# Kernel optimization log

Measured on AMD Instinct MI355X. Metric: run time of the kernel, lower is better.

Reference implementation:

```python
import jax, jax.numpy as jnp
from jax import lax
import numpy as np

IN, HID, OUT = 28, 64, 10


def _lstm_layer(x_seq, W_ih, W_hh, b_ih, b_hh):
    # x_seq: [B, T, in]; PyTorch gate order: i, f, g, o (stacked along 4H)
    B = x_seq.shape[0]
    H = W_hh.shape[1]
    # Precompute input projection for all timesteps: [B, T, 4H]
    x_proj = jnp.einsum('bti,gi->btg', x_seq, W_ih) + b_ih + b_hh

    def step(carry, xt):
        h, c = carry
        gates = xt + h @ W_hh.T  # [B, 4H]
        i, f, g, o = jnp.split(gates, 4, axis=-1)
        i = jax.nn.sigmoid(i)
        f = jax.nn.sigmoid(f)
        g = jnp.tanh(g)
        o = jax.nn.sigmoid(o)
        c = f * c + i * g
        h = o * jnp.tanh(c)
        return (h, c), h

    h0 = jnp.zeros((B, H), x_seq.dtype)
    (_, _), hs = lax.scan(step, (h0, h0), jnp.swapaxes(x_proj, 0, 1))
    return jnp.swapaxes(hs, 0, 1)  # [B, T, H]


def setup_inputs() -> dict:
    key = jax.random.key(0)
    ks = jax.random.split(key, 12)
    s_in = 1.0 / np.sqrt(HID)
    u = lambda k, shape: jax.random.uniform(k, shape, jnp.float32, -s_in, s_in)
    return {
        'x': jax.random.normal(ks[0], (16384, 1, 28, 28), jnp.float32),
        'W_ih0': u(ks[1], (4 * HID, IN)),
        'W_hh0': u(ks[2], (4 * HID, HID)),
        'b_ih0': u(ks[3], (4 * HID,)),
        'b_hh0': u(ks[4], (4 * HID,)),
        'W_ih1': u(ks[5], (4 * HID, HID)),
        'W_hh1': u(ks[6], (4 * HID, HID)),
        'b_ih1': u(ks[7], (4 * HID,)),
        'b_hh1': u(ks[8], (4 * HID,)),
        'W_lin': u(ks[9], (OUT, HID)),
        'b_lin': u(ks[10], (OUT,)),
    }


def reference(x, W_ih0, W_hh0, b_ih0, b_hh0, W_ih1, W_hh1, b_ih1, b_hh1, W_lin, b_lin):
    # (N, C, H, W) -> (N, C*H, W): sequence of rows, feature = W = 28
    x = x.reshape(x.shape[0], -1, x.shape[-1])
    h1 = _lstm_layer(x, W_ih0, W_hh0, b_ih0, b_hh0)   # [B, T, 64]
    h2 = _lstm_layer(h1, W_ih1, W_hh1, b_ih1, b_hh1)  # [B, T, 64]
    last = h2[:, -1, :]
    return last @ W_lin.T + b_lin  # [B, 10]
```

## Files before the change

### kernel.cpp

```cpp
#include <hip/hip_runtime.h>


typedef _Float16 half8 __attribute__((ext_vector_type(8)));
typedef float floatx4 __attribute__((ext_vector_type(4)));

#define NFRAG 112
#define WS_BIAS_OFF (NFRAG * 1024)
#define K2 2.8853900817779268f

#if __has_builtin(__builtin_amdgcn_exp2f)
#define EXP2(v) __builtin_amdgcn_exp2f(v)
#else
#define EXP2(v) __expf(0.6931471805599453f * (v))
#endif
#define RCP(v) __builtin_amdgcn_rcpf(v)

__global__ void prep_kernel(const float* __restrict__ Wih0, const float* __restrict__ Whh0,
                            const float* __restrict__ bih0, const float* __restrict__ bhh0,
                            const float* __restrict__ Wih1, const float* __restrict__ Whh1,
                            const float* __restrict__ bih1, const float* __restrict__ bhh1,
                            _Float16* __restrict__ wA, float* __restrict__ wBias) {
    int idx = blockIdx.x * blockDim.x + threadIdx.x;
    if (idx < NFRAG * 512) {
        int f = idx >> 9, slot = idx & 511;
        int lane = slot >> 3, j = slot & 7;
        int mt, kt, layer;
        if (f < 48) { layer = 0; mt = f / 3; kt = f % 3; }
        else        { layer = 1; int f2 = f - 48; mt = f2 >> 2; kt = f2 & 3; }
        int m = mt * 16 + (lane & 15);
        int k = kt * 32 + (lane >> 4) * 8 + j;
        int u = m >> 2, g = m & 3;
        int row = g * 64 + u;
        float v;
        if (layer == 0) {
            if (k < 28)       v = Wih0[row * 28 + k];
            else if (k == 28) v = bih0[row] + bhh0[row];
            else if (k < 32)  v = 0.f;
            else              v = Whh0[row * 64 + (k - 32)];
        } else {
            if (k < 64)       v = Wih1[row * 64 + k];
            else              v = Whh1[row * 64 + (k - 64)];
        }
        float s = (g == 2) ? K2 : -1.4426950408889634f;
        wA[idx] = (_Float16)(v * s);
    } else if (idx < NFRAG * 512 + 256) {
        int m = idx - NFRAG * 512;
        int g = m & 3;
        int row = g * 64 + (m >> 2);
        float s = (g == 2) ? K2 : -1.4426950408889634f;
        wBias[m] = (bih1[row] + bhh1[row]) * s;
    }
}

template <int N>
__device__ __forceinline__ void gate_batch(const floatx4* acc, float* c,
                                           _Float16* const* planes, const int* offs) {
    float ei[N], ef[N], eg[N], eo[N];
    #pragma unroll
    for (int i = 0; i < N; ++i) {
        floatx4 a = acc[i];
        ei[i] = EXP2(a[0]);
        ef[i] = EXP2(a[1]);
        eg[i] = EXP2(a[2]);
        eo[i] = EXP2(a[3]);
    }
    float num[N], rd[N], po[N];
    #pragma unroll
    for (int i = 0; i < N; ++i) {
        float pi = 1.0f + ei[i];
        float pf = 1.0f + ef[i];
        float pg = 1.0f + eg[i];
        po[i] = 1.0f + eo[i];
        float m = pg * pi;
        num[i] = c[i] * m + (eg[i] - 1.0f) * pf;
        rd[i]  = RCP(pf * m);
    }
    float ec[N];
    #pragma unroll
    for (int i = 0; i < N; ++i) {
        float cn = num[i] * rd[i];
        c[i] = cn;
        ec[i] = EXP2(K2 * cn);
    }
    #pragma unroll
    for (int i = 0; i < N; ++i) {
        float r2 = RCP(ec[i] * po[i] + po[i]);
        float h = (ec[i] - 1.0f) * r2;
        planes[i][offs[i]] = (_Float16)h;
    }
}

__launch_bounds__(512, 4)
__global__ void lstm_mfma(const float* __restrict__ x,
                          const _Float16* __restrict__ wA,
                          const float* __restrict__ wBias,
                          const float* __restrict__ Wlin, const float* __restrict__ blin,
                          float* __restrict__ out) {
    __shared__ __align__(16) _Float16 h0p[2][2048];
    __shared__ __align__(16) _Float16 h1p[2][2048];
    __shared__ __align__(16) _Float16 xb[2][1024];
    __shared__ float wlin_s[640];
    __shared__ float blin_s[10];

    const int lane = threadIdx.x;
    const int w    = threadIdx.y;
    const int tid  = w * 64 + lane;
    const int quad = lane >> 4;
    const int col  = lane & 15;

    half8 A0[2][3], A1[2][4];
    floatx4 bias1[2];
    int hwr[2][2];
    #pragma unroll
    for (int j = 0; j < 2; ++j) {
        const int MT = 2 * w + j;
        #pragma unroll
        for (int kt = 0; kt < 3; ++kt)
            A0[j][kt] = *(const half8*)(wA + (MT * 3 + kt) * 512 + lane * 8);
        #pragma unroll
        for (int kt = 0; kt < 4; ++kt)
            A1[j][kt] = *(const half8*)(wA + (48 + MT * 4 + kt) * 512 + lane * 8);
        const int u = MT * 4 + quad;
        bias1[j] = *(const floatx4*)(wBias + u * 4);
        #pragma unroll
        for (int in = 0; in < 2; ++in)
            hwr[j][in] = (in * 2 + (u >> 5)) * 512 + (((u >> 3) & 3) * 16 + col) * 8 + (u & 7);
    }

    int xrd[2], hrd[2][2];
    #pragma unroll
    for (int in = 0; in < 2; ++in) {
        xrd[in] = in * 512 + lane * 8;
        #pragma unroll
        for (int kt = 0; kt < 2; ++kt) hrd[kt][in] = (in * 2 + kt) * 512 + lane * 8;
    }

    const int xi = tid & 31;
    const bool xvalid = xi < 28;
    const int xbi = tid >> 5;
    const float* xg = x + (blockIdx.x * 32 + xbi) * 784 + xi;
    const int xstg = ((xi >> 3) * 16 + xbi) * 8 + (xi & 7);

    {
        ((int*)&h0p[1][0])[tid * 2 + 0] = 0;
        ((int*)&h0p[1][0])[tid * 2 + 1] = 0;
        ((int*)&h1p[1][0])[tid * 2 + 0] = 0;
        ((int*)&h1p[1][0])[tid * 2 + 1] = 0;
        float xv0 = xvalid ? xg[0] : 0.f;
        float xv1 = xvalid ? xg[16 * 784] : 0.f;
        xb[0][xstg]       = (xi == 28) ? (_Float16)1.0f : (_Float16)xv0;
        xb[0][xstg + 512] = (xi == 28) ? (_Float16)1.0f : (_Float16)xv1;
    }
    __syncthreads();

    float c0[2][2] = {{0.f, 0.f}, {0.f, 0.f}};
    float c1[2][2] = {{0.f, 0.f}, {0.f, 0.f}};

    for (int p = -1; p <= 27; ++p) {
        const int pr  = p & 1;
        const int pr1 = pr ^ 1;
        const bool doL0 = (p < 27);
        const bool doL1 = (p >= 0);

        float xn0 = 0.f, xn1 = 0.f;
        if (p <= 25 && xvalid) {
            xn0 = xg[(p + 2) * 28];
            xn1 = xg[16 * 784 + (p + 2) * 28];
        }

        half8 bx[2], bh0[2][2];
        if (doL0) {
            #pragma unroll
            for (int in = 0; in < 2; ++in)
                bx[in] = *(const half8*)&xb[pr1][xrd[in]];
        }
        #pragma unroll
        for (int kt = 0; kt < 2; ++kt)
            #pragma unroll
            for (int in = 0; in < 2; ++in)
                bh0[kt][in] = *(const half8*)&h0p[pr][hrd[kt][in]];

        floatx4 acc0[2][2], acc1[2][2];
        if (doL0) {
            #pragma unroll
            for (int j = 0; j < 2; ++j)
                #pragma unroll
                for (int in = 0; in < 2; ++in) {
                    acc0[j][in] = __builtin_amdgcn_mfma_f32_16x16x32_f16(
                                      A0[j][0], bx[in], (floatx4){0.f, 0.f, 0.f, 0.f}, 0, 0, 0);
                    #pragma unroll
                    for (int kt = 0; kt < 2; ++kt)
                        acc0[j][in] = __builtin_amdgcn_mfma_f32_16x16x32_f16(
                                          A0[j][kt + 1], bh0[kt][in], acc0[j][in], 0, 0, 0);
                }
        }
        if (doL1) {
            #pragma unroll
            for (int j = 0; j < 2; ++j)
                #pragma unroll
                for (int in = 0; in < 2; ++in) {
                    acc1[j][in] = bias1[j];
                    #pragma unroll
                    for (int kt = 0; kt < 2; ++kt)
                        acc1[j][in] = __builtin_amdgcn_mfma_f32_16x16x32_f16(
                                          A1[j][kt], bh0[kt][in], acc1[j][in], 0, 0, 0);
                }

            half8 bh1[2][2];
            #pragma unroll
            for (int kt = 0; kt < 2; ++kt)
                #pragma unroll
                for (int in = 0; in < 2; ++in)
                    bh1[kt][in] = *(const half8*)&h1p[pr1][hrd[kt][in]];
            #pragma unroll
            for (int j = 0; j < 2; ++j)
                #pragma unroll
                for (int kt = 0; kt < 2; ++kt)
                    #pragma unroll
                    for (int in = 0; in < 2; ++in)
                        acc1[j][in] = __builtin_amdgcn_mfma_f32_16x16x32_f16(
                                          A1[j][kt + 2], bh1[kt][in], acc1[j][in], 0, 0, 0);
        }

        if (doL0 && doL1) {
            floatx4 a8[8] = {acc0[0][0], acc0[0][1], acc0[1][0], acc0[1][1],
                             acc1[0][0], acc1[0][1], acc1[1][0], acc1[1][1]};
            float   cc[8] = {c0[0][0], c0[0][1], c0[1][0], c0[1][1],
                             c1[0][0], c1[0][1], c1[1][0], c1[1][1]};
            _Float16* pl[8] = {h0p[pr1], h0p[pr1], h0p[pr1], h0p[pr1],
                               h1p[pr],  h1p[pr],  h1p[pr],  h1p[pr]};
            int offs[8] = {hwr[0][0], hwr[0][1], hwr[1][0], hwr[1][1],
                           hwr[0][0], hwr[0][1], hwr[1][0], hwr[1][1]};
            gate_batch<8>(a8, cc, pl, offs);
            c0[0][0] = cc[0]; c0[0][1] = cc[1]; c0[1][0] = cc[2]; c0[1][1] = cc[3];
            c1[0][0] = cc[4]; c1[0][1] = cc[5]; c1[1][0] = cc[6]; c1[1][1] = cc[7];
        } else if (doL0) {
            floatx4 a4[4] = {acc0[0][0], acc0[0][1], acc0[1][0], acc0[1][1]};
            float   cc[4] = {c0[0][0], c0[0][1], c0[1][0], c0[1][1]};
            _Float16* pl[4] = {h0p[pr1], h0p[pr1], h0p[pr1], h0p[pr1]};
            int offs[4] = {hwr[0][0], hwr[0][1], hwr[1][0], hwr[1][1]};
            gate_batch<4>(a4, cc, pl, offs);
            c0[0][0] = cc[0]; c0[0][1] = cc[1]; c0[1][0] = cc[2]; c0[1][1] = cc[3];
        } else {
            floatx4 a4[4] = {acc1[0][0], acc1[0][1], acc1[1][0], acc1[1][1]};
            float   cc[4] = {c1[0][0], c1[0][1], c1[1][0], c1[1][1]};
            _Float16* pl[4] = {h1p[pr], h1p[pr], h1p[pr], h1p[pr]};
            int offs[4] = {hwr[0][0], hwr[0][1], hwr[1][0], hwr[1][1]};
            gate_batch<4>(a4, cc, pl, offs);
            c1[0][0] = cc[0]; c1[0][1] = cc[1]; c1[1][0] = cc[2]; c1[1][1] = cc[3];
        }

        if (p <= 25) {
            xb[pr][xstg]       = (xi == 28) ? (_Float16)1.0f : (_Float16)xn0;
            xb[pr][xstg + 512] = (xi == 28) ? (_Float16)1.0f : (_Float16)xn1;
        }
        __syncthreads();
    }

    wlin_s[tid] = Wlin[tid];
    if (tid < 128) wlin_s[512 + tid] = Wlin[512 + tid];
    if (tid < 10)  blin_s[tid] = blin[tid];
    __syncthreads();
    if (tid < 320) {
        int b = tid / 10, o = tid - b * 10;
        float a = blin_s[o];
        #pragma unroll 8
        for (int uu = 0; uu < 64; ++uu) {
            float hv = (float)h1p[1][((b >> 4) * 2 + (uu >> 5)) * 512 + (((uu >> 3) & 3) * 16 + (b & 15)) * 8 + (uu & 7)];
            a += wlin_s[o * 64 + uu] * hv;
        }
        out[(blockIdx.x * 32 + b) * 10 + o] = a;
    }
}

extern "C" void kernel_launch(void* const* d_in, const int* in_sizes, int n_in,
                              void* d_out, int out_size, void* d_ws, size_t ws_size,
                              hipStream_t stream) {
    const float* x    = (const float*)d_in[0];
    const float* Wih0 = (const float*)d_in[1];
    const float* Whh0 = (const float*)d_in[2];
    const float* bih0 = (const float*)d_in[3];
    const float* bhh0 = (const float*)d_in[4];
    const float* Wih1 = (const float*)d_in[5];
    const float* Whh1 = (const float*)d_in[6];
    const float* bih1 = (const float*)d_in[7];
    const float* bhh1 = (const float*)d_in[8];
    const float* Wlin = (const float*)d_in[9];
    const float* blin = (const float*)d_in[10];
    float* out = (float*)d_out;

    _Float16* wA    = (_Float16*)d_ws;
    float*    wBias = (float*)((char*)d_ws + WS_BIAS_OFF);

    prep_kernel<<<225, 256, 0, stream>>>(Wih0, Whh0, bih0, bhh0,
                                         Wih1, Whh1, bih1, bhh1, wA, wBias);
    lstm_mfma<<<512, dim3(64, 8), 0, stream>>>(x, wA, wBias, Wlin, blin, out);
}
```

Before: 171.6 us.

## Interleave two batch groups so gate math overlaps the other group's MFMAs

Splits each block's 32 sequences into two 16-column groups that alternate phases. In each phase the gate nonlinearities for one group run while the MFMAs for the other group are issued, so the dependent MFMA->transcendental chain of one group is hidden behind the other's work. Boundary steps are handled with keep masks and a scrap LDS buffer rather than branches, and the final layer-1 gate step is peeled out after the loop. The cost is twice as many barriers per timestep, some redundant work at the edges and more live accumulator registers.

```diff
diff --git a/kernel.cpp b/kernel.cpp
--- a/kernel.cpp
+++ b/kernel.cpp
@@ -53,7 +53,7 @@
 }
 
 template <int N>
-__device__ __forceinline__ void gate_batch(const floatx4* acc, float* c,
+__device__ __forceinline__ void gate_batch(const floatx4* acc, float* c, const bool* keep,
                                            _Float16* const* planes, const int* offs) {
     float ei[N], ef[N], eg[N], eo[N];
     #pragma unroll
@@ -79,14 +79,13 @@
     #pragma unroll
     for (int i = 0; i < N; ++i) {
         float cn = num[i] * rd[i];
-        c[i] = cn;
+        c[i] = keep[i] ? cn : 0.0f;
         ec[i] = EXP2(K2 * cn);
     }
     #pragma unroll
     for (int i = 0; i < N; ++i) {
         float r2 = RCP(ec[i] * po[i] + po[i]);
-        float h = (ec[i] - 1.0f) * r2;
-        planes[i][offs[i]] = (_Float16)h;
+        planes[i][offs[i]] = (_Float16)((ec[i] - 1.0f) * r2);
     }
 }
 
@@ -96,9 +95,10 @@
                           const float* __restrict__ wBias,
                           const float* __restrict__ Wlin, const float* __restrict__ blin,
                           float* __restrict__ out) {
-    __shared__ __align__(16) _Float16 h0p[2][2048];
-    __shared__ __align__(16) _Float16 h1p[2][2048];
-    __shared__ __align__(16) _Float16 xb[2][1024];
+    __shared__ __align__(16) _Float16 h0p[2][1024];
+    __shared__ __align__(16) _Float16 h1p[2][1024];
+    __shared__ __align__(16) _Float16 xb[2][512];
+    __shared__ __align__(16) _Float16 scrap[1024];
     __shared__ float wlin_s[640];
     __shared__ float blin_s[10];
 
@@ -110,7 +110,7 @@
 
     half8 A0[2][3], A1[2][4];
     floatx4 bias1[2];
-    int hwr[2][2];
+    int hwr[2];
     #pragma unroll
     for (int j = 0; j < 2; ++j) {
         const int MT = 2 * w + j;
@@ -122,140 +122,102 @@
             A1[j][kt] = *(const half8*)(wA + (48 + MT * 4 + kt) * 512 + lane * 8);
         const int u = MT * 4 + quad;
         bias1[j] = *(const floatx4*)(wBias + u * 4);
+        hwr[j] = (u >> 5) * 512 + (((u >> 3) & 3) * 16 + col) * 8 + (u & 7);
+    }
+
+    const int xrd = lane * 8;
+    const int hrd0 = lane * 8;
+    const int hrd1 = 512 + lane * 8;
+
+    const int ks = tid & 31;
+    const int cs = tid >> 5;
+    const bool xvalid = ks < 28;
+    const bool xone   = (ks == 28);
+    int xoff[2];
+    #pragma unroll
+    for (int g = 0; g < 2; ++g)
+        xoff[g] = (blockIdx.x * 32 + g * 16 + cs) * 784 + ks;
+    const int xstg = ((ks >> 3) * 16 + cs) * 8 + (ks & 7);
+
+    {
+        ((int*)h0p)[tid] = 0; ((int*)h0p)[tid + 512] = 0;
+        ((int*)h1p)[tid] = 0; ((int*)h1p)[tid + 512] = 0;
+        float v0 = xvalid ? x[xoff[0]] : 0.f;
+        float v1 = xvalid ? x[xoff[1]] : 0.f;
+        xb[0][xstg] = xone ? (_Float16)1.0f : (_Float16)v0;
+        xb[1][xstg] = xone ? (_Float16)1.0f : (_Float16)v1;
+    }
+    __syncthreads();
+
+    floatx4 acc0g[2][2], acc1g[2][2];
+    #pragma unroll
+    for (int g = 0; g < 2; ++g)
         #pragma unroll
-        for (int in = 0; in < 2; ++in)
-            hwr[j][in] = (in * 2 + (u >> 5)) * 512 + (((u >> 3) & 3) * 16 + col) * 8 + (u & 7);
-    }
-
-    int xrd[2], hrd[2][2];
-    #pragma unroll
-    for (int in = 0; in < 2; ++in) {
-        xrd[in] = in * 512 + lane * 8;
-        #pragma unroll
-        for (int kt = 0; kt < 2; ++kt) hrd[kt][in] = (in * 2 + kt) * 512 + lane * 8;
-    }
-
-    const int xi = tid & 31;
-    const bool xvalid = xi < 28;
-    const int xbi = tid >> 5;
-    const float* xg = x + (blockIdx.x * 32 + xbi) * 784 + xi;
-    const int xstg = ((xi >> 3) * 16 + xbi) * 8 + (xi & 7);
-
-    {
-        ((int*)&h0p[1][0])[tid * 2 + 0] = 0;
-        ((int*)&h0p[1][0])[tid * 2 + 1] = 0;
-        ((int*)&h1p[1][0])[tid * 2 + 0] = 0;
-        ((int*)&h1p[1][0])[tid * 2 + 1] = 0;
-        float xv0 = xvalid ? xg[0] : 0.f;
-        float xv1 = xvalid ? xg[16 * 784] : 0.f;
-        xb[0][xstg]       = (xi == 28) ? (_Float16)1.0f : (_Float16)xv0;
-        xb[0][xstg + 512] = (xi == 28) ? (_Float16)1.0f : (_Float16)xv1;
-    }
-    __syncthreads();
-
+        for (int j = 0; j < 2; ++j) {
+            acc0g[g][j] = (floatx4){0.f, 0.f, 0.f, 0.f};
+            acc1g[g][j] = (floatx4){0.f, 0.f, 0.f, 0.f};
+        }
     float c0[2][2] = {{0.f, 0.f}, {0.f, 0.f}};
     float c1[2][2] = {{0.f, 0.f}, {0.f, 0.f}};
 
-    for (int p = -1; p <= 27; ++p) {
-        const int pr  = p & 1;
-        const int pr1 = pr ^ 1;
-        const bool doL0 = (p < 27);
-        const bool doL1 = (p >= 0);
-
-        float xn0 = 0.f, xn1 = 0.f;
-        if (p <= 25 && xvalid) {
-            xn0 = xg[(p + 2) * 28];
-            xn1 = xg[16 * 784 + (p + 2) * 28];
-        }
-
-        half8 bx[2], bh0[2][2];
-        if (doL0) {
-            #pragma unroll
-            for (int in = 0; in < 2; ++in)
-                bx[in] = *(const half8*)&xb[pr1][xrd[in]];
-        }
-        #pragma unroll
-        for (int kt = 0; kt < 2; ++kt)
-            #pragma unroll
-            for (int in = 0; in < 2; ++in)
-                bh0[kt][in] = *(const half8*)&h0p[pr][hrd[kt][in]];
-
-        floatx4 acc0[2][2], acc1[2][2];
-        if (doL0) {
-            #pragma unroll
-            for (int j = 0; j < 2; ++j)
-                #pragma unroll
-                for (int in = 0; in < 2; ++in) {
-                    acc0[j][in] = __builtin_amdgcn_mfma_f32_16x16x32_f16(
-                                      A0[j][0], bx[in], (floatx4){0.f, 0.f, 0.f, 0.f}, 0, 0, 0);
-                    #pragma unroll
-                    for (int kt = 0; kt < 2; ++kt)
-                        acc0[j][in] = __builtin_amdgcn_mfma_f32_16x16x32_f16(
-                                          A0[j][kt + 1], bh0[kt][in], acc0[j][in], 0, 0, 0);
-                }
-        }
-        if (doL1) {
-            #pragma unroll
-            for (int j = 0; j < 2; ++j)
-                #pragma unroll
-                for (int in = 0; in < 2; ++in) {
-                    acc1[j][in] = bias1[j];
-                    #pragma unroll
-                    for (int kt = 0; kt < 2; ++kt)
-                        acc1[j][in] = __builtin_amdgcn_mfma_f32_16x16x32_f16(
-                                          A1[j][kt], bh0[kt][in], acc1[j][in], 0, 0, 0);
-                }
-
-            half8 bh1[2][2];
-            #pragma unroll
-            for (int kt = 0; kt < 2; ++kt)
-                #pragma unroll
-                for (int in = 0; in < 2; ++in)
-                    bh1[kt][in] = *(const half8*)&h1p[pr1][hrd[kt][in]];
-            #pragma unroll
-            for (int j = 0; j < 2; ++j)
-                #pragma unroll
-                for (int kt = 0; kt < 2; ++kt)
-                    #pragma unroll
-                    for (int in = 0; in < 2; ++in)
-                        acc1[j][in] = __builtin_amdgcn_mfma_f32_16x16x32_f16(
-                                          A1[j][kt + 2], bh1[kt][in], acc1[j][in], 0, 0, 0);
-        }
-
-        if (doL0 && doL1) {
-            floatx4 a8[8] = {acc0[0][0], acc0[0][1], acc0[1][0], acc0[1][1],
-                             acc1[0][0], acc1[0][1], acc1[1][0], acc1[1][1]};
-            float   cc[8] = {c0[0][0], c0[0][1], c0[1][0], c0[1][1],
-                             c1[0][0], c1[0][1], c1[1][0], c1[1][1]};
-            _Float16* pl[8] = {h0p[pr1], h0p[pr1], h0p[pr1], h0p[pr1],
-                               h1p[pr],  h1p[pr],  h1p[pr],  h1p[pr]};
-            int offs[8] = {hwr[0][0], hwr[0][1], hwr[1][0], hwr[1][1],
-                           hwr[0][0], hwr[0][1], hwr[1][0], hwr[1][1]};
-            gate_batch<8>(a8, cc, pl, offs);
-            c0[0][0] = cc[0]; c0[0][1] = cc[1]; c0[1][0] = cc[2]; c0[1][1] = cc[3];
-            c1[0][0] = cc[4]; c1[0][1] = cc[5]; c1[1][0] = cc[6]; c1[1][1] = cc[7];
-        } else if (doL0) {
-            floatx4 a4[4] = {acc0[0][0], acc0[0][1], acc0[1][0], acc0[1][1]};
-            float   cc[4] = {c0[0][0], c0[0][1], c0[1][0], c0[1][1]};
-            _Float16* pl[4] = {h0p[pr1], h0p[pr1], h0p[pr1], h0p[pr1]};
-            int offs[4] = {hwr[0][0], hwr[0][1], hwr[1][0], hwr[1][1]};
-            gate_batch<4>(a4, cc, pl, offs);
-            c0[0][0] = cc[0]; c0[0][1] = cc[1]; c0[1][0] = cc[2]; c0[1][1] = cc[3];
-        } else {
-            floatx4 a4[4] = {acc1[0][0], acc1[0][1], acc1[1][0], acc1[1][1]};
-            float   cc[4] = {c1[0][0], c1[0][1], c1[1][0], c1[1][1]};
-            _Float16* pl[4] = {h1p[pr], h1p[pr], h1p[pr], h1p[pr]};
-            int offs[4] = {hwr[0][0], hwr[0][1], hwr[1][0], hwr[1][1]};
-            gate_batch<4>(a4, cc, pl, offs);
-            c1[0][0] = cc[0]; c1[0][1] = cc[1]; c1[1][0] = cc[2]; c1[1][1] = cc[3];
-        }
-
-        if (p <= 25) {
-            xb[pr][xstg]       = (xi == 28) ? (_Float16)1.0f : (_Float16)xn0;
-            xb[pr][xstg + 512] = (xi == 28) ? (_Float16)1.0f : (_Float16)xn1;
-        }
-        __syncthreads();
-    }
+#define PHASE_BODY(GM, GG, PGATE)                                                   \
+    {                                                                               \
+        const int pg_ = (PGATE);                                                    \
+        const int tt_ = (pg_ + 2 < 27) ? (pg_ + 2) : 27;                            \
+        float xv_ = xvalid ? x[xoff[GG] + tt_ * 28] : 0.f;                          \
+        half8 bx_ = *(const half8*)&xb[GM][xrd];                                    \
+        half8 bh0_0 = *(const half8*)&h0p[GM][hrd0];                                \
+        half8 bh0_1 = *(const half8*)&h0p[GM][hrd1];                                \
+        half8 bh1_0 = *(const half8*)&h1p[GM][hrd0];                                \
+        half8 bh1_1 = *(const half8*)&h1p[GM][hrd1];                                \
+                              \
+        {                                                                           \
+            _Float16* d0 = (pg_ < 27) ? &h0p[GG][0] : scrap;                        \
+            _Float16* d1 = (pg_ >= 0) ? &h1p[GG][0] : scrap;                        \
+            const bool k0 = (pg_ >= -1), k1 = (pg_ >= 0);                           \
+            floatx4 a4[4] = {acc0g[GG][0], acc0g[GG][1], acc1g[GG][0], acc1g[GG][1]};\
+            float   cc[4] = {c0[GG][0], c0[GG][1], c1[GG][0], c1[GG][1]};           \
+            bool    kk[4] = {k0, k0, k1, k1};                                       \
+            _Float16* pl[4] = {d0, d0, d1, d1};                                     \
+            int     of[4] = {hwr[0], hwr[1], hwr[0], hwr[1]};                       \
+            gate_batch<4>(a4, cc, kk, pl, of);                                      \
+            c0[GG][0] = cc[0]; c0[GG][1] = cc[1];                                   \
+            c1[GG][0] = cc[2]; c1[GG][1] = cc[3];                                   \
+        }                                                                           \
+                                                                  \
+        _Pragma("unroll")                                                           \
+        for (int j = 0; j < 2; ++j) {                                               \
+            floatx4 a = __builtin_amdgcn_mfma_f32_16x16x32_f16(                     \
+                            A0[j][0], bx_, (floatx4){0.f, 0.f, 0.f, 0.f}, 0, 0, 0); \
+            a = __builtin_amdgcn_mfma_f32_16x16x32_f16(A0[j][1], bh0_0, a, 0, 0, 0);\
+            a = __builtin_amdgcn_mfma_f32_16x16x32_f16(A0[j][2], bh0_1, a, 0, 0, 0);\
+            acc0g[GM][j] = a;                                                       \
+            floatx4 b = bias1[j];                                                   \
+            b = __builtin_amdgcn_mfma_f32_16x16x32_f16(A1[j][0], bh0_0, b, 0, 0, 0);\
+            b = __builtin_amdgcn_mfma_f32_16x16x32_f16(A1[j][1], bh0_1, b, 0, 0, 0);\
+            b = __builtin_amdgcn_mfma_f32_16x16x32_f16(A1[j][2], bh1_0, b, 0, 0, 0);\
+            b = __builtin_amdgcn_mfma_f32_16x16x32_f16(A1[j][3], bh1_1, b, 0, 0, 0);\
+            acc1g[GM][j] = b;                                                       \
+        }                                                                           \
+        xb[GG][xstg] = xone ? (_Float16)1.0f : (_Float16)xv_;                       \
+        __syncthreads();                                                            \
+    }
+
+    for (int i = 0; i <= 28; ++i) {
+        PHASE_BODY(0, 1, i - 2)
+        PHASE_BODY(1, 0, i - 1)
+    }
+
+    {
+        _Float16* d1 = &h1p[1][0];
+        floatx4 a4[4] = {acc0g[1][0], acc0g[1][1], acc1g[1][0], acc1g[1][1]};
+        float   cc[4] = {c0[1][0], c0[1][1], c1[1][0], c1[1][1]};
+        bool    kk[4] = {false, false, true, true};
+        _Float16* pl[4] = {scrap, scrap, d1, d1};
+        int     of[4] = {hwr[0], hwr[1], hwr[0], hwr[1]};
+        gate_batch<4>(a4, cc, kk, pl, of);
+    }
+    __syncthreads();
 
     wlin_s[tid] = Wlin[tid];
     if (tid < 128) wlin_s[512 + tid] = Wlin[512 + tid];
@@ -263,10 +225,11 @@
     __syncthreads();
     if (tid < 320) {
         int b = tid / 10, o = tid - b * 10;
+        int G = b >> 4, bl = b & 15;
         float a = blin_s[o];
         #pragma unroll 8
         for (int uu = 0; uu < 64; ++uu) {
-            float hv = (float)h1p[1][((b >> 4) * 2 + (uu >> 5)) * 512 + (((uu >> 3) & 3) * 16 + (b & 15)) * 8 + (uu & 7)];
+            float hv = (float)h1p[G][(uu >> 5) * 512 + (((uu >> 3) & 3) * 16 + bl) * 8 + (uu & 7)];
             a += wlin_s[o * 64 + uu] * hv;
         }
         out[(blockIdx.x * 32 + b) * 10 + o] = a;
```

After: 179.6 us. 1.05x slower.

## Switch LSTM recurrence to 32x32x16 MFMA with swizzled shared-memory layout

Applied to the files above, without the earlier changes.

Replaces the 16x16x32 MFMA tiling (two M-tiles times two batch N-tiles per wave) with a single 32x32x16 MFMA tile per wave covering all 32 batch columns. Weight fragments, shared-memory h/x staging layout and the final linear readout are re-laid out with a swizzle so each lane writes four contiguous fp16 h values in one vector store. This cuts MFMA instruction count and scattered LDS writes per step. The cost is a 16-register accumulator per layer and a different K ordering.

```diff
diff --git a/kernel.cpp b/kernel.cpp
--- a/kernel.cpp
+++ b/kernel.cpp
@@ -1,8 +1,10 @@
 #include <hip/hip_runtime.h>
 
 
-typedef _Float16 half8 __attribute__((ext_vector_type(8)));
+typedef _Float16 half8  __attribute__((ext_vector_type(8)));
+typedef _Float16 half4v __attribute__((ext_vector_type(4)));
 typedef float floatx4 __attribute__((ext_vector_type(4)));
+typedef float f32x16  __attribute__((ext_vector_type(16)));
 
 #define NFRAG 112
 #define WS_BIAS_OFF (NFRAG * 1024)
@@ -14,6 +16,7 @@
 #define EXP2(v) __expf(0.6931471805599453f * (v))
 #endif
 #define RCP(v) __builtin_amdgcn_rcpf(v)
+#define SIG(c) ((((c) & 7) << 2) | ((c) >> 3))
 
 __global__ void prep_kernel(const float* __restrict__ Wih0, const float* __restrict__ Whh0,
                             const float* __restrict__ bih0, const float* __restrict__ bhh0,
@@ -24,22 +27,23 @@
     if (idx < NFRAG * 512) {
         int f = idx >> 9, slot = idx & 511;
         int lane = slot >> 3, j = slot & 7;
-        int mt, kt, layer;
-        if (f < 48) { layer = 0; mt = f / 3; kt = f % 3; }
-        else        { layer = 1; int f2 = f - 48; mt = f2 >> 2; kt = f2 & 3; }
-        int m = mt * 16 + (lane & 15);
-        int k = kt * 32 + (lane >> 4) * 8 + j;
-        int u = m >> 2, g = m & 3;
-        int row = g * 64 + u;
+        int w, kt, layer;
+        if (f < 48) { layer = 0; w = f / 6; kt = f % 6; }
+        else        { layer = 1; int f2 = f - 48; w = f2 >> 3; kt = f2 & 7; }
+        int r  = lane & 31;
+        int a  = r >> 3, hi = (r >> 2) & 1, g = r & 3;
+        int u  = w * 8 + 4 * hi + a;
+        int wrow = g * 64 + u;
+        int k = kt * 16 + (lane >> 5) * 8 + j;
         float v;
         if (layer == 0) {
-            if (k < 28)       v = Wih0[row * 28 + k];
-            else if (k == 28) v = bih0[row] + bhh0[row];
+            if (k < 28)       v = Wih0[wrow * 28 + k];
+            else if (k == 28) v = bih0[wrow] + bhh0[wrow];
             else if (k < 32)  v = 0.f;
-            else              v = Whh0[row * 64 + (k - 32)];
+            else              v = Whh0[wrow * 64 + (k - 32)];
         } else {
-            if (k < 64)       v = Wih1[row * 64 + k];
-            else              v = Whh1[row * 64 + (k - 64)];
+            if (k < 64)       v = Wih1[wrow * 64 + k];
+            else              v = Whh1[wrow * 64 + (k - 64)];
         }
         float s = (g == 2) ? K2 : -1.4426950408889634f;
         wA[idx] = (_Float16)(v * s);
@@ -53,16 +57,14 @@
 }
 
 template <int N>
-__device__ __forceinline__ void gate_batch(const floatx4* acc, float* c,
-                                           _Float16* const* planes, const int* offs) {
+__device__ __forceinline__ void gateN(const f32x16* accs, float* c, half4v* hout) {
     float ei[N], ef[N], eg[N], eo[N];
     #pragma unroll
     for (int i = 0; i < N; ++i) {
-        floatx4 a = acc[i];
-        ei[i] = EXP2(a[0]);
-        ef[i] = EXP2(a[1]);
-        eg[i] = EXP2(a[2]);
-        eo[i] = EXP2(a[3]);
+        ei[i] = EXP2(accs[i >> 2][4 * (i & 3) + 0]);
+        ef[i] = EXP2(accs[i >> 2][4 * (i & 3) + 1]);
+        eg[i] = EXP2(accs[i >> 2][4 * (i & 3) + 2]);
+        eo[i] = EXP2(accs[i >> 2][4 * (i & 3) + 3]);
     }
     float num[N], rd[N], po[N];
     #pragma unroll
@@ -85,9 +87,15 @@
     #pragma unroll
     for (int i = 0; i < N; ++i) {
         float r2 = RCP(ec[i] * po[i] + po[i]);
-        float h = (ec[i] - 1.0f) * r2;
-        planes[i][offs[i]] = (_Float16)h;
-    }
+        hout[i >> 2][i & 3] = (_Float16)((ec[i] - 1.0f) * r2);
+    }
+}
+
+__device__ __forceinline__ f32x16 zero16() {
+    f32x16 z;
+    #pragma unroll
+    for (int i = 0; i < 16; ++i) z[i] = 0.f;
+    return z;
 }
 
 __launch_bounds__(512, 4)
@@ -105,41 +113,34 @@
     const int lane = threadIdx.x;
     const int w    = threadIdx.y;
     const int tid  = w * 64 + lane;
-    const int quad = lane >> 4;
-    const int col  = lane & 15;
-
-    half8 A0[2][3], A1[2][4];
-    floatx4 bias1[2];
-    int hwr[2][2];
-    #pragma unroll
-    for (int j = 0; j < 2; ++j) {
-        const int MT = 2 * w + j;
-        #pragma unroll
-        for (int kt = 0; kt < 3; ++kt)
-            A0[j][kt] = *(const half8*)(wA + (MT * 3 + kt) * 512 + lane * 8);
-        #pragma unroll
-        for (int kt = 0; kt < 4; ++kt)
-            A1[j][kt] = *(const half8*)(wA + (48 + MT * 4 + kt) * 512 + lane * 8);
-        const int u = MT * 4 + quad;
-        bias1[j] = *(const floatx4*)(wBias + u * 4);
-        #pragma unroll
-        for (int in = 0; in < 2; ++in)
-            hwr[j][in] = (in * 2 + (u >> 5)) * 512 + (((u >> 3) & 3) * 16 + col) * 8 + (u & 7);
-    }
-
-    int xrd[2], hrd[2][2];
-    #pragma unroll
-    for (int in = 0; in < 2; ++in) {
-        xrd[in] = in * 512 + lane * 8;
-        #pragma unroll
-        for (int kt = 0; kt < 2; ++kt) hrd[kt][in] = (in * 2 + kt) * 512 + lane * 8;
-    }
-
-    const int xi = tid & 31;
-    const bool xvalid = xi < 28;
-    const int xbi = tid >> 5;
-    const float* xg = x + (blockIdx.x * 32 + xbi) * 784 + xi;
-    const int xstg = ((xi >> 3) * 16 + xbi) * 8 + (xi & 7);
+    const int col  = lane & 31;
+    const int hi   = lane >> 5;
+
+    half8 A0[6], A1[8];
+    #pragma unroll
+    for (int kt = 0; kt < 6; ++kt)
+        A0[kt] = *(const half8*)(wA + (w * 6 + kt) * 512 + lane * 8);
+    #pragma unroll
+    for (int kt = 0; kt < 8; ++kt)
+        A1[kt] = *(const half8*)(wA + (48 + w * 8 + kt) * 512 + lane * 8);
+
+    f32x16 bias1;
+    #pragma unroll
+    for (int a = 0; a < 4; ++a) {
+        floatx4 b = *(const floatx4*)(wBias + (w * 8 + 4 * hi + a) * 4);
+        bias1[4 * a + 0] = b[0]; bias1[4 * a + 1] = b[1];
+        bias1[4 * a + 2] = b[2]; bias1[4 * a + 3] = b[3];
+    }
+
+    const int roff = ((lane >> 5) * 32 + SIG(lane & 31)) * 8;
+    const int woff = w * 256 + SIG(col) * 8 + 4 * hi;
+
+    const int ks = tid & 31;
+    const int cs = tid >> 5;
+    const bool xvalid = ks < 28;
+    const float* xg = x + (blockIdx.x * 32 + cs) * 784 + ks;
+    const int xstg0 = (ks >> 3) * 256 + SIG(cs) * 8 + (ks & 7);
+    const int xstg1 = (ks >> 3) * 256 + SIG(cs + 16) * 8 + (ks & 7);
 
     {
         ((int*)&h0p[1][0])[tid * 2 + 0] = 0;
@@ -148,13 +149,13 @@
         ((int*)&h1p[1][0])[tid * 2 + 1] = 0;
         float xv0 = xvalid ? xg[0] : 0.f;
         float xv1 = xvalid ? xg[16 * 784] : 0.f;
-        xb[0][xstg]       = (xi == 28) ? (_Float16)1.0f : (_Float16)xv0;
-        xb[0][xstg + 512] = (xi == 28) ? (_Float16)1.0f : (_Float16)xv1;
+        xb[0][xstg0] = (ks == 28) ? (_Float16)1.0f : (_Float16)xv0;
+        xb[0][xstg1] = (ks == 28) ? (_Float16)1.0f : (_Float16)xv1;
     }
     __syncthreads();
 
-    float c0[2][2] = {{0.f, 0.f}, {0.f, 0.f}};
-    float c1[2][2] = {{0.f, 0.f}, {0.f, 0.f}};
+    float c0[4] = {0.f, 0.f, 0.f, 0.f};
+    float c1[4] = {0.f, 0.f, 0.f, 0.f};
 
     for (int p = -1; p <= 27; ++p) {
         const int pr  = p & 1;
@@ -168,91 +169,62 @@
             xn1 = xg[16 * 784 + (p + 2) * 28];
         }
 
-        half8 bx[2], bh0[2][2];
+        half8 bx[2], bh0[4];
         if (doL0) {
-            #pragma unroll
-            for (int in = 0; in < 2; ++in)
-                bx[in] = *(const half8*)&xb[pr1][xrd[in]];
+            bx[0] = *(const half8*)&xb[pr1][roff];
+            bx[1] = *(const half8*)&xb[pr1][512 + roff];
         }
         #pragma unroll
-        for (int kt = 0; kt < 2; ++kt)
-            #pragma unroll
-            for (int in = 0; in < 2; ++in)
-                bh0[kt][in] = *(const half8*)&h0p[pr][hrd[kt][in]];
-
-        floatx4 acc0[2][2], acc1[2][2];
+        for (int kt = 0; kt < 4; ++kt)
+            bh0[kt] = *(const half8*)&h0p[pr][kt * 512 + roff];
+
+        f32x16 acc0, acc1;
         if (doL0) {
-            #pragma unroll
-            for (int j = 0; j < 2; ++j)
-                #pragma unroll
-                for (int in = 0; in < 2; ++in) {
-                    acc0[j][in] = __builtin_amdgcn_mfma_f32_16x16x32_f16(
-                                      A0[j][0], bx[in], (floatx4){0.f, 0.f, 0.f, 0.f}, 0, 0, 0);
-                    #pragma unroll
-                    for (int kt = 0; kt < 2; ++kt)
-                        acc0[j][in] = __builtin_amdgcn_mfma_f32_16x16x32_f16(
-                                          A0[j][kt + 1], bh0[kt][in], acc0[j][in], 0, 0, 0);
-                }
+            acc0 = __builtin_amdgcn_mfma_f32_32x32x16_f16(A0[0], bx[0], zero16(), 0, 0, 0);
+            acc0 = __builtin_amdgcn_mfma_f32_32x32x16_f16(A0[1], bx[1], acc0, 0, 0, 0);
+            #pragma unroll
+            for (int kt = 0; kt < 4; ++kt)
+                acc0 = __builtin_amdgcn_mfma_f32_32x32x16_f16(A0[2 + kt], bh0[kt], acc0, 0, 0, 0);
         }
         if (doL1) {
-            #pragma unroll
-            for (int j = 0; j < 2; ++j)
-                #pragma unroll
-                for (int in = 0; in < 2; ++in) {
-                    acc1[j][in] = bias1[j];
-                    #pragma unroll
-                    for (int kt = 0; kt < 2; ++kt)
-                        acc1[j][in] = __builtin_amdgcn_mfma_f32_16x16x32_f16(
-                                          A1[j][kt], bh0[kt][in], acc1[j][in], 0, 0, 0);
-                }
-
-            half8 bh1[2][2];
-            #pragma unroll
-            for (int kt = 0; kt < 2; ++kt)
-                #pragma unroll
-                for (int in = 0; in < 2; ++in)
-                    bh1[kt][in] = *(const half8*)&h1p[pr1][hrd[kt][in]];
-            #pragma unroll
-            for (int j = 0; j < 2; ++j)
-                #pragma unroll
-                for (int kt = 0; kt < 2; ++kt)
-                    #pragma unroll
-                    for (int in = 0; in < 2; ++in)
-                        acc1[j][in] = __builtin_amdgcn_mfma_f32_16x16x32_f16(
-                                          A1[j][kt + 2], bh1[kt][in], acc1[j][in], 0, 0, 0);
+            acc1 = bias1;
+            #pragma unroll
+            for (int kt = 0; kt < 4; ++kt)
+                acc1 = __builtin_amdgcn_mfma_f32_32x32x16_f16(A1[kt], bh0[kt], acc1, 0, 0, 0);
+
+            half8 bh1[4];
+            #pragma unroll
+            for (int kt = 0; kt < 4; ++kt)
+                bh1[kt] = *(const half8*)&h1p[pr1][kt * 512 + roff];
+            #pragma unroll
+            for (int kt = 0; kt < 4; ++kt)
+                acc1 = __builtin_amdgcn_mfma_f32_32x32x16_f16(A1[4 + kt], bh1[kt], acc1, 0, 0, 0);
         }
 
         if (doL0 && doL1) {
-            floatx4 a8[8] = {acc0[0][0], acc0[0][1], acc0[1][0], acc0[1][1],
-                             acc1[0][0], acc1[0][1], acc1[1][0], acc1[1][1]};
-            float   cc[8] = {c0[0][0], c0[0][1], c0[1][0], c0[1][1],
-                             c1[0][0], c1[0][1], c1[1][0], c1[1][1]};
-            _Float16* pl[8] = {h0p[pr1], h0p[pr1], h0p[pr1], h0p[pr1],
-                               h1p[pr],  h1p[pr],  h1p[pr],  h1p[pr]};
-            int offs[8] = {hwr[0][0], hwr[0][1], hwr[1][0], hwr[1][1],
-                           hwr[0][0], hwr[0][1], hwr[1][0], hwr[1][1]};
-            gate_batch<8>(a8, cc, pl, offs);
-            c0[0][0] = cc[0]; c0[0][1] = cc[1]; c0[1][0] = cc[2]; c0[1][1] = cc[3];
-            c1[0][0] = cc[4]; c1[0][1] = cc[5]; c1[1][0] = cc[6]; c1[1][1] = cc[7];
+            f32x16 accs[2] = {acc0, acc1};
+            float cc[8] = {c0[0], c0[1], c0[2], c0[3], c1[0], c1[1], c1[2], c1[3]};
+            half4v h[2];
+            gateN<8>(accs, cc, h);
+            c0[0] = cc[0]; c0[1] = cc[1]; c0[2] = cc[2]; c0[3] = cc[3];
+            c1[0] = cc[4]; c1[1] = cc[5]; c1[2] = cc[6]; c1[3] = cc[7];
+            *(half4v*)&h0p[pr1][woff] = h[0];
+            *(half4v*)&h1p[pr][woff]  = h[1];
         } else if (doL0) {
-            floatx4 a4[4] = {acc0[0][0], acc0[0][1], acc0[1][0], acc0[1][1]};
-            float   cc[4] = {c0[0][0], c0[0][1], c0[1][0], c0[1][1]};
-            _Float16* pl[4] = {h0p[pr1], h0p[pr1], h0p[pr1], h0p[pr1]};
-            int offs[4] = {hwr[0][0], hwr[0][1], hwr[1][0], hwr[1][1]};
-            gate_batch<4>(a4, cc, pl, offs);
-            c0[0][0] = cc[0]; c0[0][1] = cc[1]; c0[1][0] = cc[2]; c0[1][1] = cc[3];
+            f32x16 accs[1] = {acc0};
+            half4v h[1];
+            gateN<4>(accs, c0, h);
+            *(half4v*)&h0p[pr1][woff] = h[0];
         } else {
-            floatx4 a4[4] = {acc1[0][0], acc1[0][1], acc1[1][0], acc1[1][1]};
-            float   cc[4] = {c1[0][0], c1[0][1], c1[1][0], c1[1][1]};
-            _Float16* pl[4] = {h1p[pr], h1p[pr], h1p[pr], h1p[pr]};
-            int offs[4] = {hwr[0][0], hwr[0][1], hwr[1][0], hwr[1][1]};
-            gate_batch<4>(a4, cc, pl, offs);
-            c1[0][0] = cc[0]; c1[0][1] = cc[1]; c1[1][0] = cc[2]; c1[1][1] = cc[3];
+            f32x16 accs[1] = {acc1};
+            half4v h[1];
+            gateN<4>(accs, c1, h);
+            *(half4v*)&h1p[pr][woff] = h[0];
         }
 
         if (p <= 25) {
-            xb[pr][xstg]       = (xi == 28) ? (_Float16)1.0f : (_Float16)xn0;
-            xb[pr][xstg + 512] = (xi == 28) ? (_Float16)1.0f : (_Float16)xn1;
+            xb[pr][xstg0] = (ks == 28) ? (_Float16)1.0f : (_Float16)xn0;
+            xb[pr][xstg1] = (ks == 28) ? (_Float16)1.0f : (_Float16)xn1;
         }
         __syncthreads();
     }
@@ -263,10 +235,11 @@
     __syncthreads();
     if (tid < 320) {
         int b = tid / 10, o = tid - b * 10;
+        int sb = SIG(b);
         float a = blin_s[o];
         #pragma unroll 8
         for (int uu = 0; uu < 64; ++uu) {
-            float hv = (float)h1p[1][((b >> 4) * 2 + (uu >> 5)) * 512 + (((uu >> 3) & 3) * 16 + (b & 15)) * 8 + (uu & 7)];
+            float hv = (float)h1p[1][(uu >> 3) * 256 + sb * 8 + (uu & 7)];
             a += wlin_s[o * 64 + uu] * hv;
         }
         out[(blockIdx.x * 32 + b) * 10 + o] = a;
```

After: 189.0 us. 1.1x slower.

## Halve waves per block, give each wave four M-tiles and split batch halves

Applied to the files above, without the earlier changes.

Blocks shrink from 8 to 4 waves. Each wave now holds weights for four gate M-tiles instead of two and processes the two batch halves in sequence, running the gate math on one half while the other half's MFMAs can issue. This cuts per-step barrier participants and raises per-wave work and ILP. The cost is roughly doubled weight registers per wave, lower occupancy (launch bounds 256,2), and fewer waves per CU to hide latency across the recurrent sync points.

```diff
diff --git a/kernel.cpp b/kernel.cpp
--- a/kernel.cpp
+++ b/kernel.cpp
@@ -52,21 +52,20 @@
     }
 }
 
-template <int N>
-__device__ __forceinline__ void gate_batch(const floatx4* acc, float* c,
-                                           _Float16* const* planes, const int* offs) {
-    float ei[N], ef[N], eg[N], eo[N];
-    #pragma unroll
-    for (int i = 0; i < N; ++i) {
+__device__ __forceinline__ void gate4(const floatx4* acc, float* c,
+                                      _Float16* plane, const int* offs) {
+    float ei[4], ef[4], eg[4], eo[4];
+    #pragma unroll
+    for (int i = 0; i < 4; ++i) {
         floatx4 a = acc[i];
         ei[i] = EXP2(a[0]);
         ef[i] = EXP2(a[1]);
         eg[i] = EXP2(a[2]);
         eo[i] = EXP2(a[3]);
     }
-    float num[N], rd[N], po[N];
-    #pragma unroll
-    for (int i = 0; i < N; ++i) {
+    float num[4], rd[4], po[4];
+    #pragma unroll
+    for (int i = 0; i < 4; ++i) {
         float pi = 1.0f + ei[i];
         float pf = 1.0f + ef[i];
         float pg = 1.0f + eg[i];
@@ -75,22 +74,21 @@
         num[i] = c[i] * m + (eg[i] - 1.0f) * pf;
         rd[i]  = RCP(pf * m);
     }
-    float ec[N];
-    #pragma unroll
-    for (int i = 0; i < N; ++i) {
+    float ec[4];
+    #pragma unroll
+    for (int i = 0; i < 4; ++i) {
         float cn = num[i] * rd[i];
         c[i] = cn;
         ec[i] = EXP2(K2 * cn);
     }
     #pragma unroll
-    for (int i = 0; i < N; ++i) {
+    for (int i = 0; i < 4; ++i) {
         float r2 = RCP(ec[i] * po[i] + po[i]);
-        float h = (ec[i] - 1.0f) * r2;
-        planes[i][offs[i]] = (_Float16)h;
-    }
-}
-
-__launch_bounds__(512, 4)
+        plane[offs[i]] = (_Float16)((ec[i] - 1.0f) * r2);
+    }
+}
+
+__launch_bounds__(256, 2)
 __global__ void lstm_mfma(const float* __restrict__ x,
                           const _Float16* __restrict__ wA,
                           const float* __restrict__ wBias,
@@ -107,54 +105,49 @@
     const int tid  = w * 64 + lane;
     const int quad = lane >> 4;
     const int col  = lane & 15;
-
-    half8 A0[2][3], A1[2][4];
-    floatx4 bias1[2];
-    int hwr[2][2];
-    #pragma unroll
-    for (int j = 0; j < 2; ++j) {
-        const int MT = 2 * w + j;
+    const int l8   = lane * 8;
+
+    half8 A0[4][3], A1[4][4];
+    floatx4 bias1[4];
+    int hwr0[4];
+    #pragma unroll
+    for (int j = 0; j < 4; ++j) {
+        const int MT = 4 * w + j;
         #pragma unroll
         for (int kt = 0; kt < 3; ++kt)
-            A0[j][kt] = *(const half8*)(wA + (MT * 3 + kt) * 512 + lane * 8);
+            A0[j][kt] = *(const half8*)(wA + (MT * 3 + kt) * 512 + l8);
         #pragma unroll
         for (int kt = 0; kt < 4; ++kt)
-            A1[j][kt] = *(const half8*)(wA + (48 + MT * 4 + kt) * 512 + lane * 8);
+            A1[j][kt] = *(const half8*)(wA + (48 + MT * 4 + kt) * 512 + l8);
         const int u = MT * 4 + quad;
         bias1[j] = *(const floatx4*)(wBias + u * 4);
-        #pragma unroll
-        for (int in = 0; in < 2; ++in)
-            hwr[j][in] = (in * 2 + (u >> 5)) * 512 + (((u >> 3) & 3) * 16 + col) * 8 + (u & 7);
-    }
-
-    int xrd[2], hrd[2][2];
-    #pragma unroll
-    for (int in = 0; in < 2; ++in) {
-        xrd[in] = in * 512 + lane * 8;
-        #pragma unroll
-        for (int kt = 0; kt < 2; ++kt) hrd[kt][in] = (in * 2 + kt) * 512 + lane * 8;
-    }
-
-    const int xi = tid & 31;
-    const bool xvalid = xi < 28;
-    const int xbi = tid >> 5;
-    const float* xg = x + (blockIdx.x * 32 + xbi) * 784 + xi;
-    const int xstg = ((xi >> 3) * 16 + xbi) * 8 + (xi & 7);
+        hwr0[j] = (u >> 5) * 512 + (((u >> 3) & 3) * 16 + col) * 8 + (u & 7);
+    }
+
+    const int ks = tid & 31;
+    const int cs = tid >> 5;
+    const bool xvalid = ks < 28;
+    const bool xone   = (ks == 28);
+    const float* xg = x + (blockIdx.x * 32 + cs) * 784 + ks;
+    const int xstg0 = ((ks >> 3) * 16 + cs) * 8 + (ks & 7);
 
     {
-        ((int*)&h0p[1][0])[tid * 2 + 0] = 0;
-        ((int*)&h0p[1][0])[tid * 2 + 1] = 0;
-        ((int*)&h1p[1][0])[tid * 2 + 0] = 0;
-        ((int*)&h1p[1][0])[tid * 2 + 1] = 0;
-        float xv0 = xvalid ? xg[0] : 0.f;
-        float xv1 = xvalid ? xg[16 * 784] : 0.f;
-        xb[0][xstg]       = (xi == 28) ? (_Float16)1.0f : (_Float16)xv0;
-        xb[0][xstg + 512] = (xi == 28) ? (_Float16)1.0f : (_Float16)xv1;
+        #pragma unroll
+        for (int k = 0; k < 4; ++k) {
+            ((int*)&h0p[1][0])[tid * 4 + k] = 0;
+            ((int*)&h1p[1][0])[tid * 4 + k] = 0;
+        }
+        #pragma unroll
+        for (int s = 0; s < 4; ++s) {
+            float xv = xvalid ? xg[s * 8 * 784] : 0.f;
+            xb[0][xstg0 + (s & 1) * 64 + (s >> 1) * 512] =
+                xone ? (_Float16)1.0f : (_Float16)xv;
+        }
     }
     __syncthreads();
 
-    float c0[2][2] = {{0.f, 0.f}, {0.f, 0.f}};
-    float c1[2][2] = {{0.f, 0.f}, {0.f, 0.f}};
+    float c0[2][4] = {{0.f, 0.f, 0.f, 0.f}, {0.f, 0.f, 0.f, 0.f}};
+    float c1[2][4] = {{0.f, 0.f, 0.f, 0.f}, {0.f, 0.f, 0.f, 0.f}};
 
     for (int p = -1; p <= 27; ++p) {
         const int pr  = p & 1;
@@ -162,107 +155,99 @@
         const bool doL0 = (p < 27);
         const bool doL1 = (p >= 0);
 
-        float xn0 = 0.f, xn1 = 0.f;
+        float xn[4] = {0.f, 0.f, 0.f, 0.f};
         if (p <= 25 && xvalid) {
-            xn0 = xg[(p + 2) * 28];
-            xn1 = xg[16 * 784 + (p + 2) * 28];
-        }
-
-        half8 bx[2], bh0[2][2];
-        if (doL0) {
-            #pragma unroll
-            for (int in = 0; in < 2; ++in)
-                bx[in] = *(const half8*)&xb[pr1][xrd[in]];
-        }
-        #pragma unroll
-        for (int kt = 0; kt < 2; ++kt)
-            #pragma unroll
-            for (int in = 0; in < 2; ++in)
-                bh0[kt][in] = *(const half8*)&h0p[pr][hrd[kt][in]];
-
-        floatx4 acc0[2][2], acc1[2][2];
-        if (doL0) {
-            #pragma unroll
-            for (int j = 0; j < 2; ++j)
+            const float* xgp = xg + (p + 2) * 28;
+            #pragma unroll
+            for (int s = 0; s < 4; ++s) xn[s] = xgp[s * 8 * 784];
+        }
+
+        #pragma unroll
+        for (int in = 0; in < 2; ++in) {
+            const int hb = in * 1024;
+
+            half8 bh0[2];
+            #pragma unroll
+            for (int kt = 0; kt < 2; ++kt)
+                bh0[kt] = *(const half8*)&h0p[pr][hb + kt * 512 + l8];
+
+            int offs[4];
+            #pragma unroll
+            for (int j = 0; j < 4; ++j) offs[j] = hwr0[j] + hb;
+
+            if (doL0) {
+                half8 bx = *(const half8*)&xb[pr1][in * 512 + l8];
+                floatx4 acc0[4];
                 #pragma unroll
-                for (int in = 0; in < 2; ++in) {
-                    acc0[j][in] = __builtin_amdgcn_mfma_f32_16x16x32_f16(
-                                      A0[j][0], bx[in], (floatx4){0.f, 0.f, 0.f, 0.f}, 0, 0, 0);
-                    #pragma unroll
-                    for (int kt = 0; kt < 2; ++kt)
-                        acc0[j][in] = __builtin_amdgcn_mfma_f32_16x16x32_f16(
-                                          A0[j][kt + 1], bh0[kt][in], acc0[j][in], 0, 0, 0);
+                for (int j = 0; j < 4; ++j) {
+                    acc0[j] = __builtin_amdgcn_mfma_f32_16x16x32_f16(
+                                  A0[j][0], bx, (floatx4){0.f, 0.f, 0.f, 0.f}, 0, 0, 0);
+                    #pragma unroll
+                    for (int kt = 0; kt < 2; ++kt)
+                        acc0[j] = __builtin_amdgcn_mfma_f32_16x16x32_f16(
+                                      A0[j][kt + 1], bh0[kt], acc0[j], 0, 0, 0);
                 }
-        }
-        if (doL1) {
-            #pragma unroll
-            for (int j = 0; j < 2; ++j)
-                #pragma unroll
-                for (int in = 0; in < 2; ++in) {
-                    acc1[j][in] = bias1[j];
-                    #pragma unroll
-                    for (int kt = 0; kt < 2; ++kt)
-                        acc1[j][in] = __builtin_amdgcn_mfma_f32_16x16x32_f16(
-                                          A1[j][kt], bh0[kt][in], acc1[j][in], 0, 0, 0);
+                if (doL1) {
+                    floatx4 acc1[4];
+                    half8 bh1[2];
+                    #pragma unroll
+                    for (int kt = 0; kt < 2; ++kt)
+                        bh1[kt] = *(const half8*)&h1p[pr1][hb + kt * 512 + l8];
+                    #pragma unroll
+                    for (int j = 0; j < 4; ++j) {
+                        acc1[j] = bias1[j];
+                        #pragma unroll
+                        for (int kt = 0; kt < 2; ++kt)
+                            acc1[j] = __builtin_amdgcn_mfma_f32_16x16x32_f16(
+                                          A1[j][kt], bh0[kt], acc1[j], 0, 0, 0);
+                        #pragma unroll
+                        for (int kt = 0; kt < 2; ++kt)
+                            acc1[j] = __builtin_amdgcn_mfma_f32_16x16x32_f16(
+                                          A1[j][kt + 2], bh1[kt], acc1[j], 0, 0, 0);
+                    }
+                    gate4(acc0, c0[in], &h0p[pr1][0], offs);
+                    gate4(acc1, c1[in], &h1p[pr][0], offs);
+                } else {
+                    gate4(acc0, c0[in], &h0p[pr1][0], offs);
                 }
-
-            half8 bh1[2][2];
-            #pragma unroll
-            for (int kt = 0; kt < 2; ++kt)
-                #pragma unroll
-                for (int in = 0; in < 2; ++in)
-                    bh1[kt][in] = *(const half8*)&h1p[pr1][hrd[kt][in]];
-            #pragma unroll
-            for (int j = 0; j < 2; ++j)
+            } else {
+                floatx4 acc1[4];
+                half8 bh1[2];
                 #pragma unroll
                 for (int kt = 0; kt < 2; ++kt)
-                    #pragma unroll
-                    for (int in = 0; in < 2; ++in)
-                        acc1[j][in] = __builtin_amdgcn_mfma_f32_16x16x32_f16(
-                                          A1[j][kt + 2], bh1[kt][in], acc1[j][in], 0, 0, 0);
-        }
-
-        if (doL0 && doL1) {
-            floatx4 a8[8] = {acc0[0][0], acc0[0][1], acc0[1][0], acc0[1][1],
-                             acc1[0][0], acc1[0][1], acc1[1][0], acc1[1][1]};
-            float   cc[8] = {c0[0][0], c0[0][1], c0[1][0], c0[1][1],
-                             c1[0][0], c1[0][1], c1[1][0], c1[1][1]};
-            _Float16* pl[8] = {h0p[pr1], h0p[pr1], h0p[pr1], h0p[pr1],
-                               h1p[pr],  h1p[pr],  h1p[pr],  h1p[pr]};
-            int offs[8] = {hwr[0][0], hwr[0][1], hwr[1][0], hwr[1][1],
-                           hwr[0][0], hwr[0][1], hwr[1][0], hwr[1][1]};
-            gate_batch<8>(a8, cc, pl, offs);
-            c0[0][0] = cc[0]; c0[0][1] = cc[1]; c0[1][0] = cc[2]; c0[1][1] = cc[3];
-            c1[0][0] = cc[4]; c1[0][1] = cc[5]; c1[1][0] = cc[6]; c1[1][1] = cc[7];
-        } else if (doL0) {
-            floatx4 a4[4] = {acc0[0][0], acc0[0][1], acc0[1][0], acc0[1][1]};
-            float   cc[4] = {c0[0][0], c0[0][1], c0[1][0], c0[1][1]};
-            _Float16* pl[4] = {h0p[pr1], h0p[pr1], h0p[pr1], h0p[pr1]};
-            int offs[4] = {hwr[0][0], hwr[0][1], hwr[1][0], hwr[1][1]};
-            gate_batch<4>(a4, cc, pl, offs);
-            c0[0][0] = cc[0]; c0[0][1] = cc[1]; c0[1][0] = cc[2]; c0[1][1] = cc[3];
-        } else {
-            floatx4 a4[4] = {acc1[0][0], acc1[0][1], acc1[1][0], acc1[1][1]};
-            float   cc[4] = {c1[0][0], c1[0][1], c1[1][0], c1[1][1]};
-            _Float16* pl[4] = {h1p[pr], h1p[pr], h1p[pr], h1p[pr]};
-            int offs[4] = {hwr[0][0], hwr[0][1], hwr[1][0], hwr[1][1]};
-            gate_batch<4>(a4, cc, pl, offs);
-            c1[0][0] = cc[0]; c1[0][1] = cc[1]; c1[1][0] = cc[2]; c1[1][1] = cc[3];
+                    bh1[kt] = *(const half8*)&h1p[pr1][hb + kt * 512 + l8];
+                #pragma unroll
+                for (int j = 0; j < 4; ++j) {
+                    acc1[j] = bias1[j];
+                    #pragma unroll
+                    for (int kt = 0; kt < 2; ++kt)
+                        acc1[j] = __builtin_amdgcn_mfma_f32_16x16x32_f16(
+                                      A1[j][kt], bh0[kt], acc1[j], 0, 0, 0);
+                    #pragma unroll
+                    for (int kt = 0; kt < 2; ++kt)
+                        acc1[j] = __builtin_amdgcn_mfma_f32_16x16x32_f16(
+                                      A1[j][kt + 2], bh1[kt], acc1[j], 0, 0, 0);
+                }
+                gate4(acc1, c1[in], &h1p[pr][0], offs);
+            }
         }
 
         if (p <= 25) {
-            xb[pr][xstg]       = (xi == 28) ? (_Float16)1.0f : (_Float16)xn0;
-            xb[pr][xstg + 512] = (xi == 28) ? (_Float16)1.0f : (_Float16)xn1;
+            #pragma unroll
+            for (int s = 0; s < 4; ++s)
+                xb[pr][xstg0 + (s & 1) * 64 + (s >> 1) * 512] =
+                    xone ? (_Float16)1.0f : (_Float16)xn[s];
         }
         __syncthreads();
     }
 
-    wlin_s[tid] = Wlin[tid];
-    if (tid < 128) wlin_s[512 + tid] = Wlin[512 + tid];
+    wlin_s[tid]       = Wlin[tid];
+    wlin_s[tid + 256] = Wlin[tid + 256];
+    if (tid < 128) wlin_s[tid + 512] = Wlin[tid + 512];
     if (tid < 10)  blin_s[tid] = blin[tid];
     __syncthreads();
-    if (tid < 320) {
-        int b = tid / 10, o = tid - b * 10;
+    for (int e = tid; e < 320; e += 256) {
+        int b = e / 10, o = e - b * 10;
         float a = blin_s[o];
         #pragma unroll 8
         for (int uu = 0; uu < 64; ++uu) {
@@ -294,5 +279,5 @@
 
     prep_kernel<<<225, 256, 0, stream>>>(Wih0, Whh0, bih0, bhh0,
                                          Wih1, Whh1, bih1, bhh1, wA, wBias);
-    lstm_mfma<<<512, dim3(64, 8), 0, stream>>>(x, wA, wBias, Wlin, blin, out);
-}
+    lstm_mfma<<<512, dim3(64, 4), 0, stream>>>(x, wA, wBias, Wlin, blin, out);
+}
```

Result: slower. 177.2 us (+3.3%).
